# Performance work log

Hardware: AMD Instinct MI355X
Metric: run time of the kernel (lower is better)

The kernel has to match this reference:

```python
import jax, jax.numpy as jnp
import numpy as np

B, S, E, H = 4, 2048, 1024, 128  # batch, seq_len, n_embeddings, head_size


def setup_inputs() -> dict:
    key = jax.random.key(0)
    kx, kq, kk, kv = jax.random.split(key, 4)
    x = jax.random.normal(kx, (B, S, E), dtype=jnp.float32)
    # nn.Linear(E, H, bias=False) weights, stored transposed so proj = x @ W
    Wq = jax.random.normal(kq, (E, H), dtype=jnp.float32) * 0.02
    Wk = jax.random.normal(kk, (E, H), dtype=jnp.float32) * 0.02
    Wv = jax.random.normal(kv, (E, H), dtype=jnp.float32) * 0.02
    return {"x": x, "Wq": Wq, "Wk": Wk, "Wv": Wv}


def reference(x, Wq, Wk, Wv):
    # Single causal self-attention head (dropout = identity, eval mode).
    q = jnp.einsum("bse,eh->bsh", x, Wq)  # [B,S,H]
    k = jnp.einsum("bse,eh->bsh", x, Wk)
    v = jnp.einsum("bse,eh->bsh", x, Wv)
    scale = 1.0 / jnp.sqrt(jnp.asarray(H, dtype=x.dtype))
    scores = jnp.einsum("bqh,bkh->bqk", q, k) * scale  # [B,S,S]
    causal = jnp.tril(jnp.ones((S, S), dtype=bool))
    scores = jnp.where(causal, scores, jnp.asarray(-jnp.inf, dtype=scores.dtype))
    weights = jax.nn.softmax(scores, axis=-1)
    out = jnp.einsum("bqk,bkh->bqh", weights, v)  # [B,S,H]
    return out
```

## Files before the change

### kernel.cpp

```cpp
#include <hip/hip_runtime.h>
#include <hip/hip_cooperative_groups.h>
#include <math.h>

namespace cg = cooperative_groups;

#define BB 4
#define SS 2048
#define EE 1024
#define HH 128
#define PLANE (BB * SS * HH)
#define BPLANE (SS * HH)
#define UPB_C 187
#define NU_C (UPB_C * 4)
#define NBLK_C 512
#define AUNITS 272

typedef __bf16 bf16x8 __attribute__((ext_vector_type(8)));
typedef __bf16 bf16x4 __attribute__((ext_vector_type(4)));
typedef float f32x4 __attribute__((ext_vector_type(4)));

#define QSCALE (0.08838834764831845f * 1.4426950408889634f)

__global__ __launch_bounds__(256, 2) void fused_head(
    const float* __restrict__ x, const float* __restrict__ Wq,
    const float* __restrict__ Wk, const float* __restrict__ Wv,
    __bf16* __restrict__ qkv, __bf16* __restrict__ WT,
    __bf16* __restrict__ Opart, float* __restrict__ lpart,
    float* __restrict__ out) {
  cg::grid_group grid = cg::this_grid();
  __shared__ __align__(16) char smem[35840];

  const int t = threadIdx.x, w = t >> 6, lane = t & 63;
  const int quad = lane >> 4, l16 = lane & 15;
  const int u = blockIdx.x;
  const int nb = gridDim.x;

  for (int uu = u; uu < 384; uu += nb) {
    float* LT = (float*)smem;
    const int p = uu >> 7;
    const int r0 = uu & 127;
    const int kb = (r0 >> 2) * 32, nbo = (r0 & 3) * 32;
    const float* __restrict__ W = (p == 0) ? Wq : (p == 1) ? Wk : Wv;
    const int kr = t >> 3, nc4 = (t & 7) * 4;
    const float4 v = *(const float4*)&W[(size_t)(kb + kr) * HH + nbo + nc4];
    LT[(nc4 + 0) * 33 + kr] = v.x;
    LT[(nc4 + 1) * 33 + kr] = v.y;
    LT[(nc4 + 2) * 33 + kr] = v.z;
    LT[(nc4 + 3) * 33 + kr] = v.w;
    __syncthreads();
    const int n = t >> 3, kc = (t & 7) * 4;
    bf16x4 o;
#pragma unroll
    for (int i = 0; i < 4; ++i) o[i] = (__bf16)LT[n * 33 + kc + i];
    *(bf16x4*)&WT[(size_t)p * (HH * EE) + (size_t)(nbo + n) * EE + kb + kc] = o;
    __syncthreads();
  }
  __threadfence();
  grid.sync();

  {
    const int wm = (w >> 1) * 16, wn2 = (w & 1) * 32;
    for (int uu = u; uu < 1536; uu += nb) {
      __bf16* xs = (__bf16*)smem;
      __bf16* wsd = (__bf16*)(smem + 4608);
      const int proj = uu / 512;
      const int rem = uu & 511;
      const int mb = (rem >> 1) * 32;
      const int ch = rem & 1;
      const __bf16* __restrict__ WTp =
          WT + (size_t)proj * (HH * EE) + (size_t)(ch * 64) * EE;

      const int xrow0 = t >> 4, xkc0 = (t & 15) * 4;

      f32x4 acc[2];
#pragma unroll
      for (int j = 0; j < 2; ++j) acc[j] = (f32x4){0.f, 0.f, 0.f, 0.f};

      float4 xr[2];
      bf16x8 wr[2];
#pragma unroll
      for (int i = 0; i < 2; ++i)
        xr[i] = *(const float4*)&x[(size_t)(mb + xrow0 + i * 16) * EE + xkc0];
#pragma unroll
      for (int i = 0; i < 2; ++i) {
        const int idx = t + i * 256;
        wr[i] = *(const bf16x8*)&WTp[(size_t)(idx >> 3) * EE + (idx & 7) * 8];
      }

      for (int kt = 0; kt < 16; ++kt) {
        __syncthreads();
#pragma unroll
        for (int i = 0; i < 2; ++i) {
          bf16x4 bv;
          bv[0] = (__bf16)xr[i].x; bv[1] = (__bf16)xr[i].y;
          bv[2] = (__bf16)xr[i].z; bv[3] = (__bf16)xr[i].w;
          *(bf16x4*)&xs[(xrow0 + i * 16) * 72 + xkc0] = bv;
        }
#pragma unroll
        for (int i = 0; i < 2; ++i) {
          const int idx = t + i * 256;
          *(bf16x8*)&wsd[(idx >> 3) * 72 + (idx & 7) * 8] = wr[i];
        }
        __syncthreads();

        if (kt < 15) {
          const int kb = (kt + 1) * 64;
#pragma unroll
          for (int i = 0; i < 2; ++i)
            xr[i] = *(const float4*)&x[(size_t)(mb + xrow0 + i * 16) * EE + kb + xkc0];
#pragma unroll
          for (int i = 0; i < 2; ++i) {
            const int idx = t + i * 256;
            wr[i] = *(const bf16x8*)&WTp[(size_t)(idx >> 3) * EE + kb + (idx & 7) * 8];
          }
        }

        bf16x8 af[2], bfr[2][2];
#pragma unroll
        for (int kc = 0; kc < 2; ++kc)
          af[kc] = *(const bf16x8*)&xs[(wm + l16) * 72 + kc * 32 + quad * 8];
#pragma unroll
        for (int ni = 0; ni < 2; ++ni)
#pragma unroll
          for (int kc = 0; kc < 2; ++kc)
            bfr[ni][kc] =
                *(const bf16x8*)&wsd[(wn2 + ni * 16 + l16) * 72 + kc * 32 + quad * 8];
#pragma unroll
        for (int kc = 0; kc < 2; ++kc)
#pragma unroll
          for (int ni = 0; ni < 2; ++ni)
            acc[ni] = __builtin_amdgcn_mfma_f32_16x16x32_bf16(
                af[kc], bfr[ni][kc], acc[ni], 0, 0, 0);
      }

      const int srow0 = mb + wm + quad * 4;
      if (proj < 2) {
        const float scale = (proj == 0) ? QSCALE : 1.0f;
        __bf16* outp = qkv + (size_t)proj * PLANE;
#pragma unroll
        for (int ni = 0; ni < 2; ++ni) {
          const int col = ch * 64 + wn2 + ni * 16 + l16;
#pragma unroll
          for (int rr = 0; rr < 4; ++rr)
            outp[(size_t)(srow0 + rr) * HH + col] = (__bf16)(acc[ni][rr] * scale);
        }
      } else {
        __bf16* vtp = qkv + 2 * (size_t)PLANE;
        const int bb2 = srow0 >> 11, sl = srow0 & 2047;
#pragma unroll
        for (int ni = 0; ni < 2; ++ni) {
          const int d = ch * 64 + wn2 + ni * 16 + l16;
          bf16x4 vv;
#pragma unroll
          for (int rr = 0; rr < 4; ++rr) vv[rr] = (__bf16)acc[ni][rr];
          *(bf16x4*)&vtp[(size_t)bb2 * BPLANE + (size_t)d * SS + sl] = vv;
        }
      }
      __syncthreads();
    }
  }
  __threadfence();
  grid.sync();

  for (int uu = u; uu < NU_C; uu += nb) {
    __bf16* K_s = (__bf16*)smem;
    __bf16* VT_s = (__bf16*)(smem + 17408);
    const int ur = (NU_C - 1) - uu;
    const int b = ur & 3;
    const int r = ur >> 2;
    int tt = 0, Pp = 0;
    for (;;) {
      const int n = (tt + 3) / 3;
      if (r < Pp + n) break;
      Pp += n;
      ++tt;
    }
    const int c = r - Pp;
    const int qrb = tt * 64;
    const int k0 = c * 192;
    const int kend = min(k0 + 192, qrb + 64);
    const int ntiles = (kend - k0 + 63) >> 6;
    const int qsb = qrb + w * 16;

    const size_t bq = (size_t)b * BPLANE;
    const __bf16* __restrict__ qp = qkv + bq;
    const __bf16* __restrict__ kp = qkv + PLANE + bq;
    const __bf16* __restrict__ vt = qkv + 2 * (size_t)PLANE + bq;

    bf16x8 qf[4];
#pragma unroll
    for (int cc = 0; cc < 4; ++cc)
      qf[cc] = *(const bf16x8*)&qp[(size_t)(qsb + l16) * HH + cc * 32 + quad * 8];

    f32x4 of[8];
#pragma unroll
    for (int f = 0; f < 8; ++f) of[f] = (f32x4){0.f, 0.f, 0.f, 0.f};
    float lp = 0.f;

    bf16x8 krg[4], vrg[4];
#pragma unroll
    for (int i = 0; i < 4; ++i) {
      const int idx = t + i * 256;
      const int row = idx >> 4, dc = (idx & 15) * 8;
      krg[i] = *(const bf16x8*)&kp[(size_t)(k0 + row) * HH + dc];
    }
#pragma unroll
    for (int i = 0; i < 4; ++i) {
      const int idx = t + i * 256;
      const int d = idx >> 3, kc = (idx & 7) * 8;
      vrg[i] = *(const bf16x8*)&vt[(size_t)d * SS + k0 + kc];
    }

    for (int jt = 0; jt < ntiles; ++jt) {
      __syncthreads();
#pragma unroll
      for (int i = 0; i < 4; ++i) {
        const int idx = t + i * 256;
        const int row = idx >> 4, dc = (idx & 15) * 8;
        const int lam = (row & 32) + ((row & 4) ? 16 : 0) +
                        (((row & 31) >> 3) << 2) + (row & 3);
        *(bf16x8*)&K_s[lam * 136 + dc] = krg[i];
      }
#pragma unroll
      for (int i = 0; i < 4; ++i) {
        const int idx = t + i * 256;
        const int d = idx >> 3, kc = (idx & 7) * 8;
        *(bf16x8*)&VT_s[d * 72 + kc] = vrg[i];
      }
      __syncthreads();

      if (jt + 1 < ntiles) {
        const int kb2 = k0 + (jt + 1) * 64;
#pragma unroll
        for (int i = 0; i < 4; ++i) {
          const int idx = t + i * 256;
          const int row = idx >> 4, dc = (idx & 15) * 8;
          krg[i] = *(const bf16x8*)&kp[(size_t)(kb2 + row) * HH + dc];
        }
#pragma unroll
        for (int i = 0; i < 4; ++i) {
          const int idx = t + i * 256;
          const int d = idx >> 3, kc = (idx & 7) * 8;
          vrg[i] = *(const bf16x8*)&vt[(size_t)d * SS + kb2 + kc];
        }
      }

#pragma unroll
      for (int s32 = 0; s32 < 2; ++s32) {
        const int kabs = k0 + jt * 64 + s32 * 32;
        if (kabs <= qsb + 15) {
          bf16x8 ku[4], kv[4];
#pragma unroll
          for (int cc = 0; cc < 4; ++cc) {
            ku[cc] = *(const bf16x8*)&K_s[(s32 * 32 + l16) * 136 + cc * 32 + quad * 8];
            kv[cc] = *(const bf16x8*)&K_s[(s32 * 32 + 16 + l16) * 136 + cc * 32 + quad * 8];
          }
          f32x4 su = (f32x4){0.f, 0.f, 0.f, 0.f};
          f32x4 sv = (f32x4){0.f, 0.f, 0.f, 0.f};
#pragma unroll
          for (int cc = 0; cc < 4; ++cc) {
            su = __builtin_amdgcn_mfma_f32_16x16x32_bf16(ku[cc], qf[cc], su, 0, 0, 0);
            sv = __builtin_amdgcn_mfma_f32_16x16x32_bf16(kv[cc], qf[cc], sv, 0, 0, 0);
          }
          const int qg = qsb + l16;
          bf16x8 pa;
#pragma unroll
          for (int rr = 0; rr < 4; ++rr) {
            const int kU = kabs + quad * 8 + rr;
            const float eU = (kU <= qg) ? exp2f(su[rr]) : 0.f;
            const float eV = (kU + 4 <= qg) ? exp2f(sv[rr]) : 0.f;
            pa[rr] = (__bf16)eU;
            pa[4 + rr] = (__bf16)eV;
            lp += eU + eV;
          }
#pragma unroll
          for (int f = 0; f < 8; ++f) {
            const bf16x8 vb =
                *(const bf16x8*)&VT_s[(f * 16 + l16) * 72 + s32 * 32 + quad * 8];
            of[f] = __builtin_amdgcn_mfma_f32_16x16x32_bf16(pa, vb, of[f], 0, 0, 0);
          }
        }
      }
    }

    lp += __shfl_xor(lp, 16);
    lp += __shfl_xor(lp, 32);

    if (tt < 3) {
#pragma unroll
      for (int rr = 0; rr < 4; ++rr) {
        const float lrow = __shfl(lp, quad * 4 + rr);
        const float inv = 1.0f / lrow;
#pragma unroll
        for (int f = 0; f < 8; ++f)
          out[bq + (size_t)(qsb + quad * 4 + rr) * HH + f * 16 + l16] =
              of[f][rr] * inv;
      }
    } else {
      const int us = b * UPB_C + r;
      __bf16* op = Opart + (size_t)us * 8192;
#pragma unroll
      for (int f = 0; f < 8; ++f)
#pragma unroll
        for (int rr = 0; rr < 4; ++rr)
          op[(w * 16 + quad * 4 + rr) * 128 + f * 16 + l16] = (__bf16)of[f][rr];
      if (quad == 0) lpart[us * 64 + w * 16 + l16] = lp;
    }
    __syncthreads();
  }
  __threadfence();
  grid.sync();

  for (int uu = u; uu < 464; uu += nb) {
    const int q4 = uu & 3;
    const int m = uu >> 2;
    const int b = m / 29;
    const int tile = 3 + (m % 29);
    const int nc = (tile + 3) / 3;
    int Pp = 0;
    for (int j = 0; j < tile; ++j) Pp += (j + 3) / 3;
    const int u0 = b * UPB_C + Pp;
    const int idx = q4 * 256 + t;
    const int e0 = idx * 8;
    const int row = idx >> 4;
    float acc[8] = {0.f, 0.f, 0.f, 0.f, 0.f, 0.f, 0.f, 0.f};
    float lsum = 0.f;
    for (int cc = 0; cc < nc; ++cc) {
      const bf16x8 pv = *(const bf16x8*)&Opart[(size_t)(u0 + cc) * 8192 + e0];
#pragma unroll
      for (int k = 0; k < 8; ++k) acc[k] += (float)pv[k];
      lsum += lpart[(u0 + cc) * 64 + row];
    }
    const float inv = 1.0f / lsum;
    float4 r0, r1;
    r0.x = acc[0] * inv; r0.y = acc[1] * inv; r0.z = acc[2] * inv; r0.w = acc[3] * inv;
    r1.x = acc[4] * inv; r1.y = acc[5] * inv; r1.z = acc[6] * inv; r1.w = acc[7] * inv;
    float* op = out + (size_t)b * BPLANE + (size_t)tile * 8192 + e0;
    ((float4*)op)[0] = r0;
    ((float4*)op)[1] = r1;
  }
}

__global__ __launch_bounds__(256) void prep_w(
    const float* __restrict__ Wq, const float* __restrict__ Wk,
    const float* __restrict__ Wv, __bf16* __restrict__ WT) {
  __shared__ float LT[32 * 33];
  const int p = blockIdx.x >> 7;
  const int r = blockIdx.x & 127;
  const int kb = (r >> 2) * 32, nb = (r & 3) * 32;
  const float* __restrict__ W = (p == 0) ? Wq : (p == 1) ? Wk : Wv;
  const int t = threadIdx.x;
  const int kr = t >> 3, nc4 = (t & 7) * 4;
  const float4 v = *(const float4*)&W[(size_t)(kb + kr) * HH + nb + nc4];
  LT[(nc4 + 0) * 33 + kr] = v.x;
  LT[(nc4 + 1) * 33 + kr] = v.y;
  LT[(nc4 + 2) * 33 + kr] = v.z;
  LT[(nc4 + 3) * 33 + kr] = v.w;
  __syncthreads();
  const int n = t >> 3, kc = (t & 7) * 4;
  bf16x4 o;
#pragma unroll
  for (int i = 0; i < 4; ++i) o[i] = (__bf16)LT[n * 33 + kc + i];
  *(bf16x4*)&WT[(size_t)p * (HH * EE) + (size_t)(nb + n) * EE + kb + kc] = o;
}

__global__ __launch_bounds__(256, 4) void qkv_proj(
    const float* __restrict__ x, const __bf16* __restrict__ WT,
    __bf16* __restrict__ qkv) {
  __shared__ __align__(16) __bf16 xs[32 * 72];
  __shared__ __align__(16) __bf16 wsd[128 * 72];

  const int t = threadIdx.x, w = t >> 6, lane = t & 63;
  const int quad = lane >> 4, l16 = lane & 15;
  const int mb = blockIdx.x * 32;
  const int proj = blockIdx.y;
  const __bf16* __restrict__ WTp = WT + (size_t)proj * (HH * EE);

  const int xrow0 = t >> 4, xkc0 = (t & 15) * 4;
  const int wn0 = t >> 3, wkc0 = (t & 7) * 8;

  f32x4 acc[2][2];
#pragma unroll
  for (int i = 0; i < 2; ++i)
#pragma unroll
    for (int j = 0; j < 2; ++j) acc[i][j] = (f32x4){0.f, 0.f, 0.f, 0.f};

  float4 xr[2];
  bf16x8 wr[4];
#pragma unroll
  for (int i = 0; i < 2; ++i)
    xr[i] = *(const float4*)&x[(size_t)(mb + xrow0 + i * 16) * EE + xkc0];
#pragma unroll
  for (int i = 0; i < 4; ++i)
    wr[i] = *(const bf16x8*)&WTp[(size_t)(wn0 + i * 32) * EE + wkc0];

  for (int kt = 0; kt < 16; ++kt) {
    __syncthreads();
#pragma unroll
    for (int i = 0; i < 2; ++i) {
      bf16x4 bv;
      bv[0] = (__bf16)xr[i].x; bv[1] = (__bf16)xr[i].y;
      bv[2] = (__bf16)xr[i].z; bv[3] = (__bf16)xr[i].w;
      *(bf16x4*)&xs[(xrow0 + i * 16) * 72 + xkc0] = bv;
    }
#pragma unroll
    for (int i = 0; i < 4; ++i)
      *(bf16x8*)&wsd[(wn0 + i * 32) * 72 + wkc0] = wr[i];
    __syncthreads();

    if (kt < 15) {
      const int kb = (kt + 1) * 64;
#pragma unroll
      for (int i = 0; i < 2; ++i)
        xr[i] = *(const float4*)&x[(size_t)(mb + xrow0 + i * 16) * EE + kb + xkc0];
#pragma unroll
      for (int i = 0; i < 4; ++i)
        wr[i] = *(const bf16x8*)&WTp[(size_t)(wn0 + i * 32) * EE + kb + wkc0];
    }

    bf16x8 af[2][2], bfr[2][2];
#pragma unroll
    for (int mi = 0; mi < 2; ++mi)
#pragma unroll
      for (int kc = 0; kc < 2; ++kc)
        af[mi][kc] = *(const bf16x8*)&xs[(mi * 16 + l16) * 72 + kc * 32 + quad * 8];
#pragma unroll
    for (int ni = 0; ni < 2; ++ni)
#pragma unroll
      for (int kc = 0; kc < 2; ++kc)
        bfr[ni][kc] =
            *(const bf16x8*)&wsd[(w * 32 + ni * 16 + l16) * 72 + kc * 32 + quad * 8];
#pragma unroll
    for (int kc = 0; kc < 2; ++kc)
#pragma unroll
      for (int mi = 0; mi < 2; ++mi)
#pragma unroll
        for (int ni = 0; ni < 2; ++ni)
          acc[mi][ni] = __builtin_amdgcn_mfma_f32_16x16x32_bf16(
              af[mi][kc], bfr[ni][kc], acc[mi][ni], 0, 0, 0);
  }

  if (proj < 2) {
    const float scale = (proj == 0) ? QSCALE : 1.0f;
    __bf16* outp = qkv + (size_t)proj * PLANE;
#pragma unroll
    for (int mi = 0; mi < 2; ++mi) {
      const int srow = mb + mi * 16 + quad * 4;
#pragma unroll
      for (int ni = 0; ni < 2; ++ni) {
        const int col = w * 32 + ni * 16 + l16;
#pragma unroll
        for (int rr = 0; rr < 4; ++rr)
          outp[(size_t)(srow + rr) * HH + col] = (__bf16)(acc[mi][ni][rr] * scale);
      }
    }
  } else {
    __bf16* vtp = qkv + 2 * (size_t)PLANE;
#pragma unroll
    for (int mi = 0; mi < 2; ++mi) {
      const int srow = mb + mi * 16 + quad * 4;
      const int bb2 = srow >> 11, sl = srow & 2047;
#pragma unroll
      for (int ni = 0; ni < 2; ++ni) {
        const int d = w * 32 + ni * 16 + l16;
        bf16x4 vv;
#pragma unroll
        for (int rr = 0; rr < 4; ++rr) vv[rr] = (__bf16)acc[mi][ni][rr];
        *(bf16x4*)&vtp[(size_t)bb2 * BPLANE + (size_t)d * SS + sl] = vv;
      }
    }
  }
}

__global__ __launch_bounds__(256, 3) void flash_attn_mfma(
    const __bf16* __restrict__ qkv, float* __restrict__ out,
    __bf16* __restrict__ Opart, float* __restrict__ lpart) {
  __shared__ __align__(16) __bf16 K_s[64 * 136];
  __shared__ __align__(16) __bf16 VT_s[128 * 72];

  const int t = threadIdx.x, w = t >> 6, lane = t & 63;
  const int quad = lane >> 4, l16 = lane & 15;
  const int b = blockIdx.x & 3;
  const int r = (AUNITS - 1) - (blockIdx.x >> 2);
  int tt = 0;
  while ((((tt + 2) * (tt + 2)) >> 2) <= r) ++tt;
  const int c = r - (((tt + 1) * (tt + 1)) >> 2);
  const int qrb = tt * 64;
  const int k0 = c * 128;
  const int kend = min(k0 + 128, qrb + 64);
  const int ntiles = (kend - k0) >> 6;
  const int qsb = qrb + w * 16;

  const size_t bq = (size_t)b * BPLANE;
  const __bf16* __restrict__ qp = qkv + bq;
  const __bf16* __restrict__ kp = qkv + PLANE + bq;
  const __bf16* __restrict__ vt = qkv + 2 * (size_t)PLANE + bq;

  bf16x8 qf[4];
#pragma unroll
  for (int cc = 0; cc < 4; ++cc)
    qf[cc] = *(const bf16x8*)&qp[(size_t)(qsb + l16) * HH + cc * 32 + quad * 8];

  f32x4 of[8];
#pragma unroll
  for (int f = 0; f < 8; ++f) of[f] = (f32x4){0.f, 0.f, 0.f, 0.f};
  float lp = 0.f;

  bf16x8 krg[4], vrg[4];
#pragma unroll
  for (int i = 0; i < 4; ++i) {
    const int idx = t + i * 256;
    const int row = idx >> 4, dc = (idx & 15) * 8;
    krg[i] = *(const bf16x8*)&kp[(size_t)(k0 + row) * HH + dc];
  }
#pragma unroll
  for (int i = 0; i < 4; ++i) {
    const int idx = t + i * 256;
    const int d = idx >> 3, kc = (idx & 7) * 8;
    vrg[i] = *(const bf16x8*)&vt[(size_t)d * SS + k0 + kc];
  }

  for (int jt = 0; jt < ntiles; ++jt) {
    __syncthreads();
#pragma unroll
    for (int i = 0; i < 4; ++i) {
      const int idx = t + i * 256;
      const int row = idx >> 4, dc = (idx & 15) * 8;
      const int lam = (row & 32) + ((row & 4) ? 16 : 0) +
                      (((row & 31) >> 3) << 2) + (row & 3);
      *(bf16x8*)&K_s[lam * 136 + dc] = krg[i];
    }
#pragma unroll
    for (int i = 0; i < 4; ++i) {
      const int idx = t + i * 256;
      const int d = idx >> 3, kc = (idx & 7) * 8;
      *(bf16x8*)&VT_s[d * 72 + kc] = vrg[i];
    }
    __syncthreads();

    if (jt + 1 < ntiles) {
      const int kb2 = k0 + (jt + 1) * 64;
#pragma unroll
      for (int i = 0; i < 4; ++i) {
        const int idx = t + i * 256;
        const int row = idx >> 4, dc = (idx & 15) * 8;
        krg[i] = *(const bf16x8*)&kp[(size_t)(kb2 + row) * HH + dc];
      }
#pragma unroll
      for (int i = 0; i < 4; ++i) {
        const int idx = t + i * 256;
        const int d = idx >> 3, kc = (idx & 7) * 8;
        vrg[i] = *(const bf16x8*)&vt[(size_t)d * SS + kb2 + kc];
      }
    }

#pragma unroll
    for (int s32 = 0; s32 < 2; ++s32) {
      const int kabs = k0 + jt * 64 + s32 * 32;
      if (kabs <= qsb + 15) {
        bf16x8 ku[4], kv[4];
#pragma unroll
        for (int cc = 0; cc < 4; ++cc) {
          ku[cc] = *(const bf16x8*)&K_s[(s32 * 32 + l16) * 136 + cc * 32 + quad * 8];
          kv[cc] = *(const bf16x8*)&K_s[(s32 * 32 + 16 + l16) * 136 + cc * 32 + quad * 8];
        }
        f32x4 su = (f32x4){0.f, 0.f, 0.f, 0.f};
        f32x4 sv = (f32x4){0.f, 0.f, 0.f, 0.f};
#pragma unroll
        for (int cc = 0; cc < 4; ++cc) {
          su = __builtin_amdgcn_mfma_f32_16x16x32_bf16(ku[cc], qf[cc], su, 0, 0, 0);
          sv = __builtin_amdgcn_mfma_f32_16x16x32_bf16(kv[cc], qf[cc], sv, 0, 0, 0);
        }
        const int qg = qsb + l16;
        bf16x8 pa;
#pragma unroll
        for (int rr = 0; rr < 4; ++rr) {
          const int kU = kabs + quad * 8 + rr;
          const float eU = (kU <= qg) ? exp2f(su[rr]) : 0.f;
          const float eV = (kU + 4 <= qg) ? exp2f(sv[rr]) : 0.f;
          pa[rr] = (__bf16)eU;
          pa[4 + rr] = (__bf16)eV;
          lp += eU + eV;
        }
#pragma unroll
        for (int f = 0; f < 8; ++f) {
          const bf16x8 vb =
              *(const bf16x8*)&VT_s[(f * 16 + l16) * 72 + s32 * 32 + quad * 8];
          of[f] = __builtin_amdgcn_mfma_f32_16x16x32_bf16(pa, vb, of[f], 0, 0, 0);
        }
      }
    }
  }

  lp += __shfl_xor(lp, 16);
  lp += __shfl_xor(lp, 32);

  if (tt < 2) {
#pragma unroll
    for (int rr = 0; rr < 4; ++rr) {
      const float lrow = __shfl(lp, quad * 4 + rr);
      const float inv = 1.0f / lrow;
#pragma unroll
      for (int f = 0; f < 8; ++f)
        out[bq + (size_t)(qsb + quad * 4 + rr) * HH + f * 16 + l16] =
            of[f][rr] * inv;
    }
  } else {
    const int u = b * AUNITS + r;
    __bf16* op = Opart + (size_t)u * 8192;
#pragma unroll
    for (int f = 0; f < 8; ++f)
#pragma unroll
      for (int rr = 0; rr < 4; ++rr)
        op[(w * 16 + quad * 4 + rr) * 128 + f * 16 + l16] = (__bf16)of[f][rr];
    if (quad == 0) lpart[u * 64 + w * 16 + l16] = lp;
  }
}

__global__ __launch_bounds__(256) void attn_merge(
    const __bf16* __restrict__ Opart, const float* __restrict__ lpart,
    float* __restrict__ out) {
  const int q4 = blockIdx.x & 3;
  const int m = blockIdx.x >> 2;
  const int b = m / 30;
  const int tile = 2 + (m % 30);
  const int nc = (tile + 2) >> 1;
  const int u0 = b * AUNITS + (((tile + 1) * (tile + 1)) >> 2);
  const int idx = q4 * 256 + threadIdx.x;
  const int e0 = idx * 8;
  const int row = idx >> 4;
  float acc[8] = {0.f, 0.f, 0.f, 0.f, 0.f, 0.f, 0.f, 0.f};
  float lsum = 0.f;
  for (int cc = 0; cc < nc; ++cc) {
    const bf16x8 pv = *(const bf16x8*)&Opart[(size_t)(u0 + cc) * 8192 + e0];
#pragma unroll
    for (int k = 0; k < 8; ++k) acc[k] += (float)pv[k];
    lsum += lpart[(u0 + cc) * 64 + row];
  }
  const float inv = 1.0f / lsum;
  float4 r0, r1;
  r0.x = acc[0] * inv; r0.y = acc[1] * inv; r0.z = acc[2] * inv; r0.w = acc[3] * inv;
  r1.x = acc[4] * inv; r1.y = acc[5] * inv; r1.z = acc[6] * inv; r1.w = acc[7] * inv;
  float* op = out + (size_t)b * BPLANE + (size_t)tile * 8192 + e0;
  ((float4*)op)[0] = r0;
  ((float4*)op)[1] = r1;
}

extern "C" void kernel_launch(void* const* d_in, const int* in_sizes, int n_in,
                              void* d_out, int out_size, void* d_ws, size_t ws_size,
                              hipStream_t stream) {
  const float* x  = (const float*)d_in[0];
  const float* Wq = (const float*)d_in[1];
  const float* Wk = (const float*)d_in[2];
  const float* Wv = (const float*)d_in[3];
  float* out = (float*)d_out;

  char* wsb = (char*)d_ws;
  __bf16* qkv = (__bf16*)wsb;
  __bf16* WT = (__bf16*)(wsb + (size_t)3 * PLANE * 2);
  __bf16* Opart = (__bf16*)(wsb + (size_t)3 * PLANE * 2 + (size_t)3 * HH * EE * 2);
  float* lpart = (float*)(wsb + (size_t)3 * PLANE * 2 + (size_t)3 * HH * EE * 2 +
                          (size_t)BB * AUNITS * 8192 * 2);

  int dev = 0;
  (void)hipGetDevice(&dev);
  int coop = 0, ncu = 0, maxb = 0;
  (void)hipDeviceGetAttribute(&coop, hipDeviceAttributeCooperativeLaunch, dev);
  (void)hipDeviceGetAttribute(&ncu, hipDeviceAttributeMultiprocessorCount, dev);
  (void)hipOccupancyMaxActiveBlocksPerMultiprocessor(&maxb, (const void*)fused_head,
                                                     256, 0);
  const bool use_coop = (coop != 0) && ((long)maxb * (long)ncu >= NBLK_C);

  if (use_coop) {
    void* args[] = {(void*)&x, (void*)&Wq, (void*)&Wk, (void*)&Wv,
                    (void*)&qkv, (void*)&WT, (void*)&Opart, (void*)&lpart,
                    (void*)&out};
    hipLaunchCooperativeKernel((void*)fused_head, dim3(NBLK_C), dim3(256), args,
                               0, stream);
  } else {
    prep_w<<<384, 256, 0, stream>>>(Wq, Wk, Wv, WT);
    qkv_proj<<<dim3(BB * SS / 32, 3), 256, 0, stream>>>(x, WT, qkv);
    flash_attn_mfma<<<BB * AUNITS, 256, 0, stream>>>(qkv, out, Opart, lpart);
    attn_merge<<<BB * 30 * 4, 256, 0, stream>>>(Opart, lpart, out);
  }
}
```

Baseline: 115.6 us.

## Use 128x128 attention units with two query subtiles per wave and double-buffered LDS

Reworks the attention phase so each block handles a 128-row query tile against a 128-key chunk, with every wave processing two 16-row query subtiles. Each K/V tile loaded into shared memory is therefore reused across twice as many queries. K/V shared buffers are double-buffered, leaving one barrier per tile instead of two. The partial-combine phase is adapted to the new triangular unit layout. Shared memory doubles to about 70KB, which may limit occupancy under launch_bounds(256,2), and per-thread register pressure rises.

```diff
diff --git a/kernel.cpp b/kernel.cpp
--- a/kernel.cpp
+++ b/kernel.cpp
@@ -10,8 +10,8 @@
 #define HH 128
 #define PLANE (BB * SS * HH)
 #define BPLANE (SS * HH)
-#define UPB_C 187
-#define NU_C (UPB_C * 4)
+#define UPB2 136
+#define NU2 544
 #define NBLK_C 512
 #define AUNITS 272
 
@@ -28,7 +28,7 @@
     __bf16* __restrict__ Opart, float* __restrict__ lpart,
     float* __restrict__ out) {
   cg::grid_group grid = cg::this_grid();
-  __shared__ __align__(16) char smem[35840];
+  __shared__ __align__(16) char smem[71680];
 
   const int t = threadIdx.x, w = t >> 6, lane = t & 63;
   const int quad = lane >> 4, l16 = lane & 15;
@@ -162,40 +162,39 @@
   __threadfence();
   grid.sync();
 
-  for (int uu = u; uu < NU_C; uu += nb) {
-    __bf16* K_s = (__bf16*)smem;
-    __bf16* VT_s = (__bf16*)(smem + 17408);
-    const int ur = (NU_C - 1) - uu;
+  for (int uu = u; uu < NU2; uu += nb) {
+    __bf16* K_s0 = (__bf16*)smem;
+    __bf16* VT_s0 = (__bf16*)(smem + 2 * 17408);
+    const int ur = (NU2 - 1) - uu;
     const int b = ur & 3;
     const int r = ur >> 2;
-    int tt = 0, Pp = 0;
-    for (;;) {
-      const int n = (tt + 3) / 3;
-      if (r < Pp + n) break;
-      Pp += n;
-      ++tt;
-    }
-    const int c = r - Pp;
-    const int qrb = tt * 64;
-    const int k0 = c * 192;
-    const int kend = min(k0 + 192, qrb + 64);
-    const int ntiles = (kend - k0 + 63) >> 6;
-    const int qsb = qrb + w * 16;
+    int T = 0;
+    while (((T + 1) * (T + 2)) >> 1 <= r) ++T;
+    const int c = r - ((T * (T + 1)) >> 1);
+    const int qrb = T * 128;
+    const int k0 = c * 128;
+    const int ntiles = 2;
+    const int wq = qrb + w * 32;
 
     const size_t bq = (size_t)b * BPLANE;
     const __bf16* __restrict__ qp = qkv + bq;
     const __bf16* __restrict__ kp = qkv + PLANE + bq;
     const __bf16* __restrict__ vt = qkv + 2 * (size_t)PLANE + bq;
 
-    bf16x8 qf[4];
-#pragma unroll
-    for (int cc = 0; cc < 4; ++cc)
-      qf[cc] = *(const bf16x8*)&qp[(size_t)(qsb + l16) * HH + cc * 32 + quad * 8];
-
-    f32x4 of[8];
-#pragma unroll
-    for (int f = 0; f < 8; ++f) of[f] = (f32x4){0.f, 0.f, 0.f, 0.f};
-    float lp = 0.f;
+    bf16x8 qf[2][4];
+#pragma unroll
+    for (int sub = 0; sub < 2; ++sub)
+#pragma unroll
+      for (int cc = 0; cc < 4; ++cc)
+        qf[sub][cc] = *(const bf16x8*)&qp[(size_t)(wq + sub * 16 + l16) * HH +
+                                          cc * 32 + quad * 8];
+
+    f32x4 of[2][8];
+#pragma unroll
+    for (int sub = 0; sub < 2; ++sub)
+#pragma unroll
+      for (int f = 0; f < 8; ++f) of[sub][f] = (f32x4){0.f, 0.f, 0.f, 0.f};
+    float lp[2] = {0.f, 0.f};
 
     bf16x8 krg[4], vrg[4];
 #pragma unroll
@@ -210,24 +209,26 @@
       const int d = idx >> 3, kc = (idx & 7) * 8;
       vrg[i] = *(const bf16x8*)&vt[(size_t)d * SS + k0 + kc];
     }
+#pragma unroll
+    for (int i = 0; i < 4; ++i) {
+      const int idx = t + i * 256;
+      const int row = idx >> 4, dc = (idx & 15) * 8;
+      const int lam = (row & 32) + ((row & 4) ? 16 : 0) +
+                      (((row & 31) >> 3) << 2) + (row & 3);
+      *(bf16x8*)&K_s0[lam * 136 + dc] = krg[i];
+    }
+#pragma unroll
+    for (int i = 0; i < 4; ++i) {
+      const int idx = t + i * 256;
+      const int d = idx >> 3, kc = (idx & 7) * 8;
+      *(bf16x8*)&VT_s0[d * 72 + kc] = vrg[i];
+    }
+    __syncthreads();
 
     for (int jt = 0; jt < ntiles; ++jt) {
-      __syncthreads();
-#pragma unroll
-      for (int i = 0; i < 4; ++i) {
-        const int idx = t + i * 256;
-        const int row = idx >> 4, dc = (idx & 15) * 8;
-        const int lam = (row & 32) + ((row & 4) ? 16 : 0) +
-                        (((row & 31) >> 3) << 2) + (row & 3);
-        *(bf16x8*)&K_s[lam * 136 + dc] = krg[i];
-      }
-#pragma unroll
-      for (int i = 0; i < 4; ++i) {
-        const int idx = t + i * 256;
-        const int d = idx >> 3, kc = (idx & 7) * 8;
-        *(bf16x8*)&VT_s[d * 72 + kc] = vrg[i];
-      }
-      __syncthreads();
+      const int cur = jt & 1;
+      __bf16* K_s = K_s0 + cur * 8704;
+      __bf16* VT_s = VT_s0 + cur * 9216;
 
       if (jt + 1 < ntiles) {
         const int kb2 = k0 + (jt + 1) * 64;
@@ -248,94 +249,130 @@
 #pragma unroll
       for (int s32 = 0; s32 < 2; ++s32) {
         const int kabs = k0 + jt * 64 + s32 * 32;
-        if (kabs <= qsb + 15) {
+        if (kabs <= wq + 31) {
           bf16x8 ku[4], kv[4];
 #pragma unroll
           for (int cc = 0; cc < 4; ++cc) {
             ku[cc] = *(const bf16x8*)&K_s[(s32 * 32 + l16) * 136 + cc * 32 + quad * 8];
             kv[cc] = *(const bf16x8*)&K_s[(s32 * 32 + 16 + l16) * 136 + cc * 32 + quad * 8];
           }
-          f32x4 su = (f32x4){0.f, 0.f, 0.f, 0.f};
-          f32x4 sv = (f32x4){0.f, 0.f, 0.f, 0.f};
-#pragma unroll
-          for (int cc = 0; cc < 4; ++cc) {
-            su = __builtin_amdgcn_mfma_f32_16x16x32_bf16(ku[cc], qf[cc], su, 0, 0, 0);
-            sv = __builtin_amdgcn_mfma_f32_16x16x32_bf16(kv[cc], qf[cc], sv, 0, 0, 0);
-          }
-          const int qg = qsb + l16;
-          bf16x8 pa;
-#pragma unroll
-          for (int rr = 0; rr < 4; ++rr) {
-            const int kU = kabs + quad * 8 + rr;
-            const float eU = (kU <= qg) ? exp2f(su[rr]) : 0.f;
-            const float eV = (kU + 4 <= qg) ? exp2f(sv[rr]) : 0.f;
-            pa[rr] = (__bf16)eU;
-            pa[4 + rr] = (__bf16)eV;
-            lp += eU + eV;
+          f32x4 su[2] = {(f32x4){0.f, 0.f, 0.f, 0.f}, (f32x4){0.f, 0.f, 0.f, 0.f}};
+          f32x4 sv[2] = {(f32x4){0.f, 0.f, 0.f, 0.f}, (f32x4){0.f, 0.f, 0.f, 0.f}};
+#pragma unroll
+          for (int cc = 0; cc < 4; ++cc)
+#pragma unroll
+            for (int sub = 0; sub < 2; ++sub) {
+              su[sub] = __builtin_amdgcn_mfma_f32_16x16x32_bf16(ku[cc], qf[sub][cc], su[sub], 0, 0, 0);
+              sv[sub] = __builtin_amdgcn_mfma_f32_16x16x32_bf16(kv[cc], qf[sub][cc], sv[sub], 0, 0, 0);
+            }
+          bf16x8 pa[2];
+#pragma unroll
+          for (int sub = 0; sub < 2; ++sub) {
+            const int qg = wq + sub * 16 + l16;
+#pragma unroll
+            for (int rr = 0; rr < 4; ++rr) {
+              const int kU = kabs + quad * 8 + rr;
+              const float eU = (kU <= qg) ? exp2f(su[sub][rr]) : 0.f;
+              const float eV = (kU + 4 <= qg) ? exp2f(sv[sub][rr]) : 0.f;
+              pa[sub][rr] = (__bf16)eU;
+              pa[sub][4 + rr] = (__bf16)eV;
+              lp[sub] += eU + eV;
+            }
           }
 #pragma unroll
           for (int f = 0; f < 8; ++f) {
             const bf16x8 vb =
                 *(const bf16x8*)&VT_s[(f * 16 + l16) * 72 + s32 * 32 + quad * 8];
-            of[f] = __builtin_amdgcn_mfma_f32_16x16x32_bf16(pa, vb, of[f], 0, 0, 0);
+#pragma unroll
+            for (int sub = 0; sub < 2; ++sub)
+              of[sub][f] = __builtin_amdgcn_mfma_f32_16x16x32_bf16(pa[sub], vb, of[sub][f], 0, 0, 0);
           }
         }
       }
-    }
-
-    lp += __shfl_xor(lp, 16);
-    lp += __shfl_xor(lp, 32);
-
-    if (tt < 3) {
-#pragma unroll
-      for (int rr = 0; rr < 4; ++rr) {
-        const float lrow = __shfl(lp, quad * 4 + rr);
-        const float inv = 1.0f / lrow;
+
+      if (jt + 1 < ntiles) {
+        const int nxt = cur ^ 1;
+        __bf16* K_n = K_s0 + nxt * 8704;
+        __bf16* VT_n = VT_s0 + nxt * 9216;
+#pragma unroll
+        for (int i = 0; i < 4; ++i) {
+          const int idx = t + i * 256;
+          const int row = idx >> 4, dc = (idx & 15) * 8;
+          const int lam = (row & 32) + ((row & 4) ? 16 : 0) +
+                          (((row & 31) >> 3) << 2) + (row & 3);
+          *(bf16x8*)&K_n[lam * 136 + dc] = krg[i];
+        }
+#pragma unroll
+        for (int i = 0; i < 4; ++i) {
+          const int idx = t + i * 256;
+          const int d = idx >> 3, kc = (idx & 7) * 8;
+          *(bf16x8*)&VT_n[d * 72 + kc] = vrg[i];
+        }
+      }
+      __syncthreads();
+    }
+
+#pragma unroll
+    for (int sub = 0; sub < 2; ++sub) {
+      lp[sub] += __shfl_xor(lp[sub], 16);
+      lp[sub] += __shfl_xor(lp[sub], 32);
+    }
+
+    if (T == 0) {
+#pragma unroll
+      for (int sub = 0; sub < 2; ++sub)
+#pragma unroll
+        for (int rr = 0; rr < 4; ++rr) {
+          const float lrow = __shfl(lp[sub], quad * 4 + rr);
+          const float inv = 1.0f / lrow;
+#pragma unroll
+          for (int f = 0; f < 8; ++f)
+            out[bq + (size_t)(wq + sub * 16 + quad * 4 + rr) * HH + f * 16 + l16] =
+                of[sub][f][rr] * inv;
+        }
+    } else {
+      const int us = b * UPB2 + r;
+      __bf16* op = Opart + (size_t)us * 16384;
+#pragma unroll
+      for (int sub = 0; sub < 2; ++sub)
 #pragma unroll
         for (int f = 0; f < 8; ++f)
-          out[bq + (size_t)(qsb + quad * 4 + rr) * HH + f * 16 + l16] =
-              of[f][rr] * inv;
-      }
-    } else {
-      const int us = b * UPB_C + r;
-      __bf16* op = Opart + (size_t)us * 8192;
-#pragma unroll
-      for (int f = 0; f < 8; ++f)
-#pragma unroll
-        for (int rr = 0; rr < 4; ++rr)
-          op[(w * 16 + quad * 4 + rr) * 128 + f * 16 + l16] = (__bf16)of[f][rr];
-      if (quad == 0) lpart[us * 64 + w * 16 + l16] = lp;
-    }
-    __syncthreads();
+#pragma unroll
+          for (int rr = 0; rr < 4; ++rr)
+            op[(w * 32 + sub * 16 + quad * 4 + rr) * 128 + f * 16 + l16] =
+                (__bf16)of[sub][f][rr];
+      if (quad == 0) {
+        lpart[us * 128 + w * 32 + l16] = lp[0];
+        lpart[us * 128 + w * 32 + 16 + l16] = lp[1];
+      }
+    }
   }
   __threadfence();
   grid.sync();
 
-  for (int uu = u; uu < 464; uu += nb) {
-    const int q4 = uu & 3;
-    const int m = uu >> 2;
-    const int b = m / 29;
-    const int tile = 3 + (m % 29);
-    const int nc = (tile + 3) / 3;
-    int Pp = 0;
-    for (int j = 0; j < tile; ++j) Pp += (j + 3) / 3;
-    const int u0 = b * UPB_C + Pp;
-    const int idx = q4 * 256 + t;
+  for (int uu = u; uu < 480; uu += nb) {
+    const int seg = uu & 7;
+    const int m = uu >> 3;
+    const int b = m / 15;
+    const int T = 1 + (m % 15);
+    const int nc = T + 1;
+    const int u0 = b * UPB2 + ((T * (T + 1)) >> 1);
+    const int idx = seg * 256 + t;
     const int e0 = idx * 8;
     const int row = idx >> 4;
     float acc[8] = {0.f, 0.f, 0.f, 0.f, 0.f, 0.f, 0.f, 0.f};
     float lsum = 0.f;
     for (int cc = 0; cc < nc; ++cc) {
-      const bf16x8 pv = *(const bf16x8*)&Opart[(size_t)(u0 + cc) * 8192 + e0];
+      const bf16x8 pv = *(const bf16x8*)&Opart[(size_t)(u0 + cc) * 16384 + e0];
 #pragma unroll
       for (int k = 0; k < 8; ++k) acc[k] += (float)pv[k];
-      lsum += lpart[(u0 + cc) * 64 + row];
+      lsum += lpart[(u0 + cc) * 128 + row];
     }
     const float inv = 1.0f / lsum;
     float4 r0, r1;
     r0.x = acc[0] * inv; r0.y = acc[1] * inv; r0.z = acc[2] * inv; r0.w = acc[3] * inv;
     r1.x = acc[4] * inv; r1.y = acc[5] * inv; r1.z = acc[6] * inv; r1.w = acc[7] * inv;
-    float* op = out + (size_t)b * BPLANE + (size_t)tile * 8192 + e0;
+    float* op = out + (size_t)b * BPLANE + (size_t)T * 16384 + e0;
     ((float4*)op)[0] = r0;
     ((float4*)op)[1] = r1;
   }
```

Result: no change. 116.3 us (+0.6%).
